# Performance work log

Hardware: AMD Instinct MI355X
Metric: run time of the kernel (lower is better)

The kernel has to match this reference:

```python
import jax, jax.numpy as jnp
import numpy as np

NUM_HEADS = 16
EPS = 1e-05


def setup_inputs() -> dict:
    key = jax.random.key(0)
    k1, k2, k3 = jax.random.split(key, 3)
    b, n, d = 2, 2048, 1024
    x = jax.random.normal(k1, (b, n, d), dtype=jnp.float32)
    # nn.Linear weights stored here as (in, out); scaled like typical init
    wqkv = jax.random.normal(k2, (d, 3 * d), dtype=jnp.float32) * (1.0 / np.sqrt(d))
    wo = jax.random.normal(k3, (d, d), dtype=jnp.float32) * (1.0 / np.sqrt(d))
    return {"x": x, "wqkv": wqkv, "wo": wo}


def reference(x, wqkv, wo):
    b, n, d = x.shape
    h = NUM_HEADS
    hd = d // h
    qkv = x @ wqkv                      # (b, n, 3d)
    q, k, v = jnp.split(qkv, 3, axis=-1)
    q = jax.nn.relu(q)
    k = jax.nn.relu(k)
    # (b, n, h*hd) -> (b, h, n, hd)
    split_heads = lambda t: t.reshape(b, n, h, hd).transpose(0, 2, 1, 3)
    q, k, v = split_heads(q), split_heads(k), split_heads(v)
    # cumulative outer products: kv[b,h,t] = sum_{s<=t} k_s (x) v_s  -> (b,h,n,hd,hd)
    kv = jnp.cumsum(k[..., :, None] * v[..., None, :], axis=2)
    num = jnp.einsum('bhnd,bhnde->bhne', q, kv)          # (b, h, n, hd)
    k_sum = jnp.cumsum(k, axis=2)                        # (b, h, n, hd)
    den = jnp.einsum('bhnd,bhnd->bhn', q, k_sum)[..., None] + EPS
    y = num / den                                        # (b, h, n, hd)
    y = y.transpose(0, 2, 1, 3).reshape(b, n, d)         # merge heads
    return y @ wo
```

## Files before the change

### kernel.cpp

```cpp
#include <hip/hip_runtime.h>
#include <hip/hip_bf16.h>

#define SEQ    2048
#define DMODEL 1024
#define NHEADS 16
#define HD     64
#define CS     64
#define NC     (SEQ / CS)
#define STSZ   (HD * HD + HD)
#define EPS_LA 1e-5f
#define LP     72
#define CLP    136

typedef __attribute__((ext_vector_type(8))) short  bf16x8;
typedef __attribute__((ext_vector_type(8))) unsigned short ushort8;
typedef __attribute__((ext_vector_type(4))) float  f32x4;

__device__ __forceinline__ void gload_lds16(const void* g, void* l) {
  __builtin_amdgcn_global_load_lds(
      (const __attribute__((address_space(1))) void*)g,
      (__attribute__((address_space(3))) void*)l, 16, 0, 0);
}

__device__ __forceinline__ ushort f2bf(float x) {
  __hip_bfloat16 h = __float2bfloat16(x);
  return __builtin_bit_cast(ushort, h);
}
__device__ __forceinline__ float bf2f(ushort u) {
  unsigned int v = ((unsigned int)u) << 16;
  return __builtin_bit_cast(float, v);
}

__device__ __forceinline__ void transpose_tile(
    const float* __restrict__ src, ushort* __restrict__ dst,
    int R, int Ncols, int r0, int c0, float (*t)[65], int tid) {
  const int lr = tid >> 2;
  const int lc = (tid & 3) * 16;
  const float* sp = src + (size_t)(r0 + lr) * Ncols + c0 + lc;
  #pragma unroll
  for (int j = 0; j < 4; ++j) {
    float4 v = *(const float4*)(sp + j * 4);
    t[lr][lc + j * 4 + 0] = v.x;
    t[lr][lc + j * 4 + 1] = v.y;
    t[lr][lc + j * 4 + 2] = v.z;
    t[lr][lc + j * 4 + 3] = v.w;
  }
  __syncthreads();
  ushort out[16];
  #pragma unroll
  for (int j = 0; j < 16; ++j)
    out[j] = f2bf(t[lc + j][lr]);
  ushort* dp = dst + (size_t)(c0 + lr) * R + r0 + lc;
  *(uint4*)dp = *(const uint4*)&out[0];
  *(uint4*)(dp + 8) = *(const uint4*)&out[8];
}

__global__ __launch_bounds__(256) void prep(
    const float* __restrict__ x, const float* __restrict__ wqkv,
    const float* __restrict__ wo, ushort* __restrict__ xb,
    ushort* __restrict__ wqkvT, ushort* __restrict__ woT) {
  __shared__ float t[64][65];
  const int bid = blockIdx.x;
  const int tid = threadIdx.x;
  if (bid < 4096) {
    const int i = bid * 256 + tid;
    float4 v = *(const float4*)(x + (size_t)i * 4);
    ushort4 o;
    o.x = f2bf(v.x); o.y = f2bf(v.y); o.z = f2bf(v.z); o.w = f2bf(v.w);
    *(ushort4*)(xb + (size_t)i * 4) = o;
  } else if (bid < 4096 + 768) {
    const int b2 = bid - 4096;
    const int bx = b2 % 48, by = b2 / 48;
    transpose_tile(wqkv, wqkvT, DMODEL, 3 * DMODEL, by * 64, bx * 64, t, tid);
  } else {
    const int b3 = bid - 4096 - 768;
    const int bx = b3 % 16, by = b3 / 16;
    transpose_tile(wo, woT, DMODEL, DMODEL, by * 64, bx * 64, t, tid);
  }
}

__global__ __launch_bounds__(256) void gemm_b16(
    const ushort* __restrict__ A, const ushort* __restrict__ Bt,
    ushort* __restrict__ C, int M, int N, int K, int relu_limit) {
  __shared__ ushort sh[128 * CLP];
  ushort* Asm = sh;
  ushort* Bsm = sh + 128 * 64;

  const int tid  = threadIdx.x;
  const int lane = tid & 63;
  const int w    = tid >> 6;
  const int wr   = w >> 1, wc = w & 1;
  const int brow = blockIdx.y * 128;
  const int bcol = blockIdx.x * 128;

  f32x4 acc[4][4];
  #pragma unroll
  for (int i = 0; i < 4; ++i)
    #pragma unroll
    for (int j = 0; j < 4; ++j) acc[i][j] = (f32x4)0.f;

  const int r8   = lane >> 3;
  const int arow = w * 32 + r8;
  const int acol = ((lane & 7) ^ r8) * 8;
  const ushort* Ag = A  + (size_t)(brow + arow) * K + acol;
  const ushort* Bg = Bt + (size_t)(bcol + arow) * K + acol;

  const int l15 = lane & 15;
  const int khi = (lane >> 4) * 8;

  for (int k0 = 0; k0 < K; k0 += 64) {
    #pragma unroll
    for (int u = 0; u < 4; ++u) {
      gload_lds16(Ag + k0 + (size_t)u * 8 * K, &Asm[(w * 4 + u) * 512]);
      gload_lds16(Bg + k0 + (size_t)u * 8 * K, &Bsm[(w * 4 + u) * 512]);
    }
    __syncthreads();
    #pragma unroll
    for (int kk = 0; kk < 2; ++kk) {
      const int ko = kk * 32 + khi;
      bf16x8 af[4], bfr[4];
      #pragma unroll
      for (int mi = 0; mi < 4; ++mi) {
        const int row = wr * 64 + mi * 16 + l15;
        af[mi] = *(const bf16x8*)&Asm[row * 64 + (ko ^ ((row & 7) << 3))];
      }
      #pragma unroll
      for (int ni = 0; ni < 4; ++ni) {
        const int row = wc * 64 + ni * 16 + l15;
        bfr[ni] = *(const bf16x8*)&Bsm[row * 64 + (ko ^ ((row & 7) << 3))];
      }
      #pragma unroll
      for (int mi = 0; mi < 4; ++mi)
        #pragma unroll
        for (int ni = 0; ni < 4; ++ni)
          acc[mi][ni] = __builtin_amdgcn_mfma_f32_16x16x32_bf16(
              af[mi], bfr[ni], acc[mi][ni], 0, 0, 0);
    }
    __syncthreads();
  }

  #pragma unroll
  for (int mi = 0; mi < 4; ++mi) {
    #pragma unroll
    for (int ni = 0; ni < 4; ++ni) {
      const int row0 = wr * 64 + mi * 16 + (lane >> 4) * 4;
      const int col  = wc * 64 + ni * 16 + l15;
      const bool rl  = bcol + col < relu_limit;
      #pragma unroll
      for (int i = 0; i < 4; ++i) {
        float v = acc[mi][ni][i];
        if (rl) v = fmaxf(v, 0.f);
        sh[(row0 + i) * CLP + col] = f2bf(v);
      }
    }
  }
  __syncthreads();
  const int r    = tid >> 1;
  const int cseg = (tid & 1) * 64;
  ushort* dst = C + (size_t)(brow + r) * N + bcol + cseg;
  const ushort* srcp = &sh[r * CLP + cseg];
  #pragma unroll
  for (int j = 0; j < 8; ++j)
    *(ushort8*)(dst + j * 8) = *(const ushort8*)(srcp + j * 8);
}

__global__ __launch_bounds__(256) void gemm_f32(
    const ushort* __restrict__ A, const ushort* __restrict__ Bt,
    float* __restrict__ C, int M, int N, int K, int relu_limit) {
  __shared__ ushort Asm[128 * 64];
  __shared__ ushort Bsm[128 * 64];

  const int tid  = threadIdx.x;
  const int lane = tid & 63;
  const int w    = tid >> 6;
  const int wr   = w >> 1, wc = w & 1;
  const int brow = blockIdx.y * 128;
  const int bcol = blockIdx.x * 128;

  f32x4 acc[4][4];
  #pragma unroll
  for (int i = 0; i < 4; ++i)
    #pragma unroll
    for (int j = 0; j < 4; ++j) acc[i][j] = (f32x4)0.f;

  const int r8   = lane >> 3;
  const int arow = w * 32 + r8;
  const int acol = ((lane & 7) ^ r8) * 8;
  const ushort* Ag = A  + (size_t)(brow + arow) * K + acol;
  const ushort* Bg = Bt + (size_t)(bcol + arow) * K + acol;

  const int l15 = lane & 15;
  const int khi = (lane >> 4) * 8;

  for (int k0 = 0; k0 < K; k0 += 64) {
    #pragma unroll
    for (int u = 0; u < 4; ++u) {
      gload_lds16(Ag + k0 + (size_t)u * 8 * K, &Asm[(w * 4 + u) * 512]);
      gload_lds16(Bg + k0 + (size_t)u * 8 * K, &Bsm[(w * 4 + u) * 512]);
    }
    __syncthreads();
    #pragma unroll
    for (int kk = 0; kk < 2; ++kk) {
      const int ko = kk * 32 + khi;
      bf16x8 af[4], bfr[4];
      #pragma unroll
      for (int mi = 0; mi < 4; ++mi) {
        const int row = wr * 64 + mi * 16 + l15;
        af[mi] = *(const bf16x8*)&Asm[row * 64 + (ko ^ ((row & 7) << 3))];
      }
      #pragma unroll
      for (int ni = 0; ni < 4; ++ni) {
        const int row = wc * 64 + ni * 16 + l15;
        bfr[ni] = *(const bf16x8*)&Bsm[row * 64 + (ko ^ ((row & 7) << 3))];
      }
      #pragma unroll
      for (int mi = 0; mi < 4; ++mi)
        #pragma unroll
        for (int ni = 0; ni < 4; ++ni)
          acc[mi][ni] = __builtin_amdgcn_mfma_f32_16x16x32_bf16(
              af[mi], bfr[ni], acc[mi][ni], 0, 0, 0);
    }
    __syncthreads();
  }

  #pragma unroll
  for (int mi = 0; mi < 4; ++mi) {
    #pragma unroll
    for (int ni = 0; ni < 4; ++ni) {
      const int r0  = brow + wr * 64 + mi * 16 + (lane >> 4) * 4;
      const int col = bcol + wc * 64 + ni * 16 + l15;
      const bool rl = col < relu_limit;
      #pragma unroll
      for (int i = 0; i < 4; ++i) {
        float v = acc[mi][ni][i];
        if (rl) v = fmaxf(v, 0.f);
        C[(size_t)(r0 + i) * N + col] = v;
      }
    }
  }
}

__global__ __launch_bounds__(256) void chunk_sums_mfma(
    const ushort* __restrict__ qkvb, ushort* __restrict__ state) {
  __shared__ ushort Kt[64 * LP];
  __shared__ ushort Vt[64 * LP];

  const int bh = blockIdx.x >> 5;
  const int c  = blockIdx.x & (NC - 1);
  const int b  = bh >> 4;
  const int h  = bh & (NHEADS - 1);
  const int tid = threadIdx.x;

  const size_t rs   = 3 * DMODEL;
  const size_t base = ((size_t)(b * SEQ + c * CS)) * rs + (size_t)h * HD;

  const int r  = tid >> 2;
  const int sg = (tid & 3) * 16;
  {
    const ushort* src = qkvb + base + (size_t)r * rs + sg;
    ushort8 k0 = *(const ushort8*)(src + DMODEL);
    ushort8 k1 = *(const ushort8*)(src + DMODEL + 8);
    ushort8 v0 = *(const ushort8*)(src + 2 * DMODEL);
    ushort8 v1 = *(const ushort8*)(src + 2 * DMODEL + 8);
    #pragma unroll
    for (int j = 0; j < 8; ++j) {
      Kt[(sg + j) * LP + r]     = k0[j];
      Kt[(sg + 8 + j) * LP + r] = k1[j];
      Vt[(sg + j) * LP + r]     = v0[j];
      Vt[(sg + 8 + j) * LP + r] = v1[j];
    }
  }
  __syncthreads();

  const int lane = tid & 63;
  const int w    = tid >> 6;
  const int l15  = lane & 15;
  const int khi  = (lane >> 4) * 8;

  bf16x8 va[2];
  #pragma unroll
  for (int kk = 0; kk < 2; ++kk)
    va[kk] = *(const bf16x8*)&Vt[(w * 16 + l15) * LP + kk * 32 + khi];

  f32x4 a[4];
  #pragma unroll
  for (int ct = 0; ct < 4; ++ct) {
    a[ct] = (f32x4)0.f;
    #pragma unroll
    for (int kk = 0; kk < 2; ++kk)
      a[ct] = __builtin_amdgcn_mfma_f32_16x16x32_bf16(
          va[kk], *(const bf16x8*)&Kt[(ct * 16 + l15) * LP + kk * 32 + khi],
          a[ct], 0, 0, 0);
  }

  ushort* st = state + (size_t)blockIdx.x * STSZ;
  #pragma unroll
  for (int ct = 0; ct < 4; ++ct) {
    #pragma unroll
    for (int i = 0; i < 4; ++i) {
      const int e = w * 16 + (lane >> 4) * 4 + i;
      const int d = ct * 16 + l15;
      st[e * HD + d] = f2bf(a[ct][i]);
    }
  }

  if (tid < HD) {
    float s = 0.f;
    #pragma unroll 8
    for (int t = 0; t < CS; ++t) s += bf2f(Kt[tid * LP + t]);
    st[HD * HD + tid] = f2bf(s);
  }
}

__global__ __launch_bounds__(256) void chunk_prefix(ushort* __restrict__ state) {
  const int g = blockIdx.x * 256 + threadIdx.x;
  const int total = 2 * NHEADS * STSZ;
  if (g >= total) return;
  const int bh   = g / STSZ;
  const int elem = g - bh * STSZ;
  ushort* p = state + (size_t)bh * NC * STSZ + elem;

  float run = 0.f;
  #pragma unroll
  for (int c = 0; c < NC; ++c) {
    const float t = bf2f(p[(size_t)c * STSZ]);
    p[(size_t)c * STSZ] = f2bf(run);
    run += t;
  }
}

__global__ __launch_bounds__(256) void chunk_out_mfma(
    const ushort* __restrict__ qkvb, const ushort* __restrict__ state,
    ushort* __restrict__ y) {
  __shared__ ushort Qs[64 * LP];
  __shared__ ushort Ks[64 * LP];
  __shared__ ushort Vt[80 * LP];
  __shared__ ushort Kv[80 * LP];
  __shared__ ushort Sm[64 * LP];

  const int bh = blockIdx.x >> 5;
  const int c  = blockIdx.x & (NC - 1);
  const int b  = bh >> 4;
  const int h  = bh & (NHEADS - 1);
  const int tid = threadIdx.x;

  const size_t rs   = 3 * DMODEL;
  const size_t base = ((size_t)(b * SEQ + c * CS)) * rs + (size_t)h * HD;

  {
    const int r  = tid >> 2;
    const int sg = (tid & 3) * 16;
    const ushort* src = qkvb + base + (size_t)r * rs + sg;
    ushort8 q0 = *(const ushort8*)(src);
    ushort8 q1 = *(const ushort8*)(src + 8);
    ushort8 k0 = *(const ushort8*)(src + DMODEL);
    ushort8 k1 = *(const ushort8*)(src + DMODEL + 8);
    ushort8 v0 = *(const ushort8*)(src + 2 * DMODEL);
    ushort8 v1 = *(const ushort8*)(src + 2 * DMODEL + 8);
    *(ushort8*)&Qs[r * LP + sg]     = q0;
    *(ushort8*)&Qs[r * LP + sg + 8] = q1;
    *(ushort8*)&Ks[r * LP + sg]     = k0;
    *(ushort8*)&Ks[r * LP + sg + 8] = k1;
    #pragma unroll
    for (int j = 0; j < 8; ++j) {
      Vt[(sg + j) * LP + r]     = v0[j];
      Vt[(sg + 8 + j) * LP + r] = v1[j];
    }
  }
  {
    const int idx = tid * 4;
    const int row = 64 + (idx >> 6);
    const int col = idx & 63;
    const ushort val = (row == 64) ? (ushort)0x3F80 : (ushort)0;
    ushort4 v4 = {val, val, val, val};
    *(ushort4*)&Vt[row * LP + col] = v4;
  }
  {
    const ushort* sp = state + ((size_t)bh * NC + c) * STSZ;
    const int off = tid * 16;
    const int e   = off >> 6;
    const int col = off & 63;
    *(ushort8*)&Kv[e * LP + col]     = *(const ushort8*)(sp + off);
    *(ushort8*)&Kv[e * LP + col + 8] = *(const ushort8*)(sp + off + 8);
    if (tid < 16) {
      const int c4 = tid * 4;
      *(ushort4*)&Kv[64 * LP + c4] = *(const ushort4*)(sp + HD * HD + c4);
    }
    if (tid < 240) {
      const int idx = tid * 4;
      const int row = 65 + (idx >> 6);
      const int col2 = idx & 63;
      ushort4 z = {0, 0, 0, 0};
      *(ushort4*)&Kv[row * LP + col2] = z;
    }
  }
  __syncthreads();

  const int lane = tid & 63;
  const int w    = tid >> 6;
  const int l15  = lane & 15;
  const int khi  = (lane >> 4) * 8;

  bf16x8 qa[2];
  #pragma unroll
  for (int kk = 0; kk < 2; ++kk)
    qa[kk] = *(const bf16x8*)&Qs[(w * 16 + l15) * LP + kk * 32 + khi];

  {
    f32x4 sac[4];
    #pragma unroll
    for (int ct = 0; ct < 4; ++ct) {
      sac[ct] = (f32x4)0.f;
      #pragma unroll
      for (int kk = 0; kk < 2; ++kk)
        sac[ct] = __builtin_amdgcn_mfma_f32_16x16x32_bf16(
            qa[kk], *(const bf16x8*)&Ks[(ct * 16 + l15) * LP + kk * 32 + khi],
            sac[ct], 0, 0, 0);
    }
    const int t0 = w * 16 + (lane >> 4) * 4;
    #pragma unroll
    for (int ct = 0; ct < 4; ++ct) {
      const int s = ct * 16 + l15;
      #pragma unroll
      for (int i = 0; i < 4; ++i) {
        const int t = t0 + i;
        const float v = (s <= t) ? sac[ct][i] : 0.f;
        Sm[t * LP + s] = f2bf(v);
      }
    }
  }
  __syncthreads();

  bf16x8 sa[2];
  #pragma unroll
  for (int kk = 0; kk < 2; ++kk)
    sa[kk] = *(const bf16x8*)&Sm[(w * 16 + l15) * LP + kk * 32 + khi];

  f32x4 o[5];
  #pragma unroll
  for (int ct = 0; ct < 5; ++ct) {
    o[ct] = (f32x4)0.f;
    #pragma unroll
    for (int kk = 0; kk < 2; ++kk)
      o[ct] = __builtin_amdgcn_mfma_f32_16x16x32_bf16(
          qa[kk], *(const bf16x8*)&Kv[(ct * 16 + l15) * LP + kk * 32 + khi],
          o[ct], 0, 0, 0);
    #pragma unroll
    for (int kk = 0; kk < 2; ++kk)
      o[ct] = __builtin_amdgcn_mfma_f32_16x16x32_bf16(
          sa[kk], *(const bf16x8*)&Vt[(ct * 16 + l15) * LP + kk * 32 + khi],
          o[ct], 0, 0, 0);
  }

  float den[4];
  #pragma unroll
  for (int i = 0; i < 4; ++i)
    den[i] = __shfl(o[4][i], lane & 48) + EPS_LA;

  const int t0 = w * 16 + (lane >> 4) * 4;
  #pragma unroll
  for (int ct = 0; ct < 4; ++ct) {
    const int e = ct * 16 + l15;
    #pragma unroll
    for (int i = 0; i < 4; ++i) {
      const int t = t0 + i;
      y[((size_t)(b * SEQ + c * CS + t)) * DMODEL + (size_t)h * HD + e] =
          f2bf(o[ct][i] / den[i]);
    }
  }
}

extern "C" void kernel_launch(void* const* d_in, const int* in_sizes, int n_in,
                              void* d_out, int out_size, void* d_ws,
                              size_t ws_size, hipStream_t stream) {
  (void)in_sizes; (void)n_in; (void)out_size; (void)ws_size;
  const float* x    = (const float*)d_in[0];
  const float* wqkv = (const float*)d_in[1];
  const float* wo   = (const float*)d_in[2];
  float* out = (float*)d_out;

  const int M  = 2 * SEQ;
  const int K  = DMODEL;
  const int N1 = 3 * DMODEL;
  const int N2 = DMODEL;

  ushort* stateb = (ushort*)d_ws;
  ushort* qkvb   = stateb + (size_t)2 * NHEADS * NC * STSZ;
  ushort* xb     = qkvb + (size_t)M * N1;
  ushort* yb     = xb + (size_t)M * K;
  ushort* wqkvT  = yb + (size_t)M * K;
  ushort* woT    = wqkvT + (size_t)K * N1;

  dim3 blk(256);

  prep<<<dim3(4096 + 768 + 256), blk, 0, stream>>>(x, wqkv, wo, xb, wqkvT, woT);

  gemm_b16<<<dim3(N1 / 128, M / 128), blk, 0, stream>>>(
      xb, wqkvT, qkvb, M, N1, K, 2 * DMODEL);

  chunk_sums_mfma<<<dim3(2 * NHEADS * NC), blk, 0, stream>>>(qkvb, stateb);

  const int total = 2 * NHEADS * STSZ;
  chunk_prefix<<<dim3((total + 255) / 256), blk, 0, stream>>>(stateb);

  chunk_out_mfma<<<dim3(2 * NHEADS * NC), blk, 0, stream>>>(qkvb, stateb, yb);

  gemm_f32<<<dim3(N2 / 128, M / 128), blk, 0, stream>>>(
      yb, woT, out, M, N2, K, 0);
}
```

Before: 95.49 us.

## Fuse fp32-to-bf16 conversion of x into QKV GEMM A-tile loads

Removes the separate x conversion pass from the prep kernel. The QKV GEMM now reads fp32 x directly, converts it to bf16 in registers and stores it into LDS, replacing the async global-to-LDS load for A. The LDS-staged coalesced epilogue is also replaced with direct scattered bf16 stores to global memory. The aim is to save one full read and write of x and a workspace buffer, at the cost of doubled A-tile global bytes per GEMM tile (re-read across 24 column blocks), synchronous loads, and less coalesced output stores.

```diff
diff --git a/kernel.cpp b/kernel.cpp
--- a/kernel.cpp
+++ b/kernel.cpp
@@ -10,7 +10,6 @@
 #define STSZ   (HD * HD + HD)
 #define EPS_LA 1e-5f
 #define LP     72
-#define CLP    136
 
 typedef __attribute__((ext_vector_type(8))) short  bf16x8;
 typedef __attribute__((ext_vector_type(8))) unsigned short ushort8;
@@ -56,35 +55,26 @@
 }
 
 __global__ __launch_bounds__(256) void prep(
-    const float* __restrict__ x, const float* __restrict__ wqkv,
-    const float* __restrict__ wo, ushort* __restrict__ xb,
+    const float* __restrict__ wqkv, const float* __restrict__ wo,
     ushort* __restrict__ wqkvT, ushort* __restrict__ woT) {
   __shared__ float t[64][65];
   const int bid = blockIdx.x;
   const int tid = threadIdx.x;
-  if (bid < 4096) {
-    const int i = bid * 256 + tid;
-    float4 v = *(const float4*)(x + (size_t)i * 4);
-    ushort4 o;
-    o.x = f2bf(v.x); o.y = f2bf(v.y); o.z = f2bf(v.z); o.w = f2bf(v.w);
-    *(ushort4*)(xb + (size_t)i * 4) = o;
-  } else if (bid < 4096 + 768) {
-    const int b2 = bid - 4096;
-    const int bx = b2 % 48, by = b2 / 48;
+  if (bid < 768) {
+    const int bx = bid % 48, by = bid / 48;
     transpose_tile(wqkv, wqkvT, DMODEL, 3 * DMODEL, by * 64, bx * 64, t, tid);
   } else {
-    const int b3 = bid - 4096 - 768;
+    const int b3 = bid - 768;
     const int bx = b3 % 16, by = b3 / 16;
     transpose_tile(wo, woT, DMODEL, DMODEL, by * 64, bx * 64, t, tid);
   }
 }
 
-__global__ __launch_bounds__(256) void gemm_b16(
-    const ushort* __restrict__ A, const ushort* __restrict__ Bt,
+__global__ __launch_bounds__(256) void gemm_x_b16(
+    const float* __restrict__ Xf, const ushort* __restrict__ Bt,
     ushort* __restrict__ C, int M, int N, int K, int relu_limit) {
-  __shared__ ushort sh[128 * CLP];
-  ushort* Asm = sh;
-  ushort* Bsm = sh + 128 * 64;
+  __shared__ ushort Asm[128 * 64];
+  __shared__ ushort Bsm[128 * 64];
 
   const int tid  = threadIdx.x;
   const int lane = tid & 63;
@@ -102,7 +92,7 @@
   const int r8   = lane >> 3;
   const int arow = w * 32 + r8;
   const int acol = ((lane & 7) ^ r8) * 8;
-  const ushort* Ag = A  + (size_t)(brow + arow) * K + acol;
+  const float*  Ag = Xf + (size_t)(brow + arow) * K + acol;
   const ushort* Bg = Bt + (size_t)(bcol + arow) * K + acol;
 
   const int l15 = lane & 15;
@@ -110,9 +100,17 @@
 
   for (int k0 = 0; k0 < K; k0 += 64) {
     #pragma unroll
+    for (int u = 0; u < 4; ++u)
+      gload_lds16(Bg + k0 + (size_t)u * 8 * K, &Bsm[(w * 4 + u) * 512]);
+    #pragma unroll
     for (int u = 0; u < 4; ++u) {
-      gload_lds16(Ag + k0 + (size_t)u * 8 * K, &Asm[(w * 4 + u) * 512]);
-      gload_lds16(Bg + k0 + (size_t)u * 8 * K, &Bsm[(w * 4 + u) * 512]);
+      const float* src = Ag + k0 + (size_t)u * 8 * K;
+      float4 f0 = *(const float4*)src;
+      float4 f1 = *(const float4*)(src + 4);
+      ushort8 p;
+      p[0] = f2bf(f0.x); p[1] = f2bf(f0.y); p[2] = f2bf(f0.z); p[3] = f2bf(f0.w);
+      p[4] = f2bf(f1.x); p[5] = f2bf(f1.y); p[6] = f2bf(f1.z); p[7] = f2bf(f1.w);
+      *(ushort8*)&Asm[(w * 4 + u) * 512 + lane * 8] = p;
     }
     __syncthreads();
     #pragma unroll
@@ -143,25 +141,17 @@
   for (int mi = 0; mi < 4; ++mi) {
     #pragma unroll
     for (int ni = 0; ni < 4; ++ni) {
-      const int row0 = wr * 64 + mi * 16 + (lane >> 4) * 4;
-      const int col  = wc * 64 + ni * 16 + l15;
-      const bool rl  = bcol + col < relu_limit;
+      const int r0  = brow + wr * 64 + mi * 16 + (lane >> 4) * 4;
+      const int col = bcol + wc * 64 + ni * 16 + l15;
+      const bool rl = col < relu_limit;
       #pragma unroll
       for (int i = 0; i < 4; ++i) {
         float v = acc[mi][ni][i];
         if (rl) v = fmaxf(v, 0.f);
-        sh[(row0 + i) * CLP + col] = f2bf(v);
-      }
-    }
-  }
-  __syncthreads();
-  const int r    = tid >> 1;
-  const int cseg = (tid & 1) * 64;
-  ushort* dst = C + (size_t)(brow + r) * N + bcol + cseg;
-  const ushort* srcp = &sh[r * CLP + cseg];
-  #pragma unroll
-  for (int j = 0; j < 8; ++j)
-    *(ushort8*)(dst + j * 8) = *(const ushort8*)(srcp + j * 8);
+        C[(size_t)(r0 + i) * N + col] = f2bf(v);
+      }
+    }
+  }
 }
 
 __global__ __launch_bounds__(256) void gemm_f32(
@@ -486,17 +476,16 @@
 
   ushort* stateb = (ushort*)d_ws;
   ushort* qkvb   = stateb + (size_t)2 * NHEADS * NC * STSZ;
-  ushort* xb     = qkvb + (size_t)M * N1;
-  ushort* yb     = xb + (size_t)M * K;
+  ushort* yb     = qkvb + (size_t)M * N1;
   ushort* wqkvT  = yb + (size_t)M * K;
   ushort* woT    = wqkvT + (size_t)K * N1;
 
   dim3 blk(256);
 
-  prep<<<dim3(4096 + 768 + 256), blk, 0, stream>>>(x, wqkv, wo, xb, wqkvT, woT);
-
-  gemm_b16<<<dim3(N1 / 128, M / 128), blk, 0, stream>>>(
-      xb, wqkvT, qkvb, M, N1, K, 2 * DMODEL);
+  prep<<<dim3(768 + 256), blk, 0, stream>>>(wqkv, wo, wqkvT, woT);
+
+  gemm_x_b16<<<dim3(N1 / 128, M / 128), blk, 0, stream>>>(
+      x, wqkvT, qkvb, M, N1, K, 2 * DMODEL);
 
   chunk_sums_mfma<<<dim3(2 * NHEADS * NC), blk, 0, stream>>>(qkvb, stateb);
 
```

Result: faster. 92.80 us (-2.8%).
